# Optimization experiments

Measured on AMD Instinct MI355X. Metric: run time of the kernel, lower is better.

The kernel has to match this reference:

```python
import jax, jax.numpy as jnp
import numpy as np

GROUPS = 32
EPS = 1e-5

def setup_inputs() -> dict:
    key = jax.random.key(0)
    ks = jax.random.split(key, 3)
    b, c, h, w = 4, 256, 64, 64
    x = jax.random.normal(ks[0], (b, c, h, w), dtype=jnp.float32)
    gn_w = jnp.ones((c,), jnp.float32)
    gn_b = jnp.zeros((c,), jnp.float32)
    qkv_w = jax.random.normal(ks[1], (3 * c, c), jnp.float32) * (1.0 / np.sqrt(c))
    qkv_b = jnp.zeros((3 * c,), jnp.float32)
    out_w = jax.random.normal(ks[2], (c, c), jnp.float32) * (1.0 / np.sqrt(c))
    out_b = jnp.zeros((c,), jnp.float32)
    return {"x": x, "gn_w": gn_w, "gn_b": gn_b, "qkv_w": qkv_w,
            "qkv_b": qkv_b, "out_w": out_w, "out_b": out_b}

def reference(x, gn_w, gn_b, qkv_w, qkv_b, out_w, out_b):
    b, c, h, w = x.shape
    scale = c ** (-0.5)
    # GroupNorm over (c/groups, h, w) per group, per-channel affine
    xg = x.reshape(b, GROUPS, c // GROUPS, h, w)
    mean = xg.mean(axis=(2, 3, 4), keepdims=True)
    var = xg.var(axis=(2, 3, 4), keepdims=True)
    xn = ((xg - mean) * jax.lax.rsqrt(var + EPS)).reshape(b, c, h, w)
    xn = xn * gn_w[None, :, None, None] + gn_b[None, :, None, None]
    # 1x1 conv to qkv: [b,3c,h,w]
    qkv = jnp.einsum('bchw,oc->bohw', xn, qkv_w) + qkv_b[None, :, None, None]
    q, k, v = jnp.split(qkv, 3, axis=1)
    # hw_to_seq: [b,c,h,w] -> [b, n, c]
    to_seq = lambda t: t.reshape(b, c, h * w).transpose(0, 2, 1)
    q, k, v = to_seq(q), to_seq(k), to_seq(v)
    sim = jnp.einsum('bic,bjc->bij', q, k) * scale  # [b,n,n]
    attn = jax.nn.softmax(sim, axis=-1)
    out = jnp.einsum('bij,bjc->bic', attn, v)  # [b,n,c]
    out = out.transpose(0, 2, 1).reshape(b, c, h, w)
    out = jnp.einsum('bchw,oc->bohw', out, out_w) + out_b[None, :, None, None]
    return out + x
```

## Files before the change

kernel.cpp:

```cpp
#include <hip/hip_runtime.h>
#include <hip/hip_bf16.h>
#include <stdint.h>

typedef __attribute__((ext_vector_type(8))) short bf16x8;
typedef __attribute__((ext_vector_type(4))) float f32x4;
typedef __attribute__((ext_vector_type(16))) float f32x16;

typedef __attribute__((address_space(1))) const uint32_t gu32;
typedef __attribute__((address_space(3))) uint32_t lu32;

#define N_PIX 4096
#define C_CH  256
#define KVB   128
#define SCALE_LOG2E (0.0625f * 1.4426950408889634f)

__device__ __forceinline__ unsigned short f2bf(float f) {
    unsigned int u = __float_as_uint(f);
    unsigned int r = (u + 0x7FFFu + ((u >> 16) & 1u)) >> 16;
    return (unsigned short)r;
}
__device__ __forceinline__ float bf2f(short s) {
    return __uint_as_float(((unsigned int)(unsigned short)s) << 16);
}

__global__ void prep_kernel(const float* __restrict__ x,
                            const float* __restrict__ gn_w,
                            const float* __restrict__ gn_b,
                            const float* __restrict__ qkv_w,
                            const float* __restrict__ out_w,
                            float* __restrict__ a_out,
                            float* __restrict__ b_out,
                            unsigned short* __restrict__ wq,
                            unsigned short* __restrict__ w2) {
    int bid = blockIdx.x;
    if (bid >= 128) {
        int i = (bid - 128) * 256 + threadIdx.x;
        wq[i] = f2bf(qkv_w[i]);
        if (i < 65536) w2[i] = f2bf(out_w[i]);
        return;
    }
    int b = bid >> 5, g = bid & 31;
    const float* base = x + ((size_t)(b * C_CH + g * 8)) * N_PIX;
    float s1 = 0.f, s2 = 0.f;
    for (int i = threadIdx.x; i < 8 * N_PIX; i += 256) {
        float v = base[i];
        s1 += v; s2 += v * v;
    }
    __shared__ float r1[256], r2[256];
    r1[threadIdx.x] = s1; r2[threadIdx.x] = s2;
    __syncthreads();
    for (int off = 128; off > 0; off >>= 1) {
        if (threadIdx.x < off) {
            r1[threadIdx.x] += r1[threadIdx.x + off];
            r2[threadIdx.x] += r2[threadIdx.x + off];
        }
        __syncthreads();
    }
    if (threadIdx.x < 8) {
        float mean = r1[0] * (1.f / 32768.f);
        float var  = r2[0] * (1.f / 32768.f) - mean * mean;
        float rstd = rsqrtf(var + 1e-5f);
        int c = g * 8 + threadIdx.x;
        float A = rstd * gn_w[c];
        a_out[b * C_CH + c] = A;
        b_out[b * C_CH + c] = gn_b[c] - mean * A;
    }
}

__global__ __launch_bounds__(256)
void qkv_gemm_kernel(const float* __restrict__ x,
                     const float* __restrict__ a_arr,
                     const float* __restrict__ bb_arr,
                     const unsigned short* __restrict__ wq,
                     const float* __restrict__ qkv_b,
                     unsigned short* __restrict__ q_seq,
                     unsigned short* __restrict__ k_seq,
                     unsigned short* __restrict__ vT) {
    __shared__ char wlds[2][16384];
    int pb   = blockIdx.x;
    int och  = blockIdx.y;
    int b    = blockIdx.z;
    int tid  = threadIdx.x;
    int wave = tid >> 6;
    int lane = tid & 63;
    int lo = lane & 15, hi = lane >> 4;
    int prow = pb * 64 + wave * 16 + lo;
    const float* xb = x + (size_t)b * C_CH * N_PIX;
    const float* av = a_arr + b * C_CH;
    const float* bv = bb_arr + b * C_CH;

    auto stageW = [&](int buf, int ks) {
#pragma unroll
        for (int pass = 0; pass < 4; pass++) {
            int chunk = pass * 256 + tid;
            int r = chunk >> 2, cslot = chunk & 3;
            const char* src = (const char*)wq + (size_t)(och * 256 + r) * 512
                              + ks * 64 + cslot * 16;
            __builtin_amdgcn_global_load_lds((gu32*)src,
                                             (lu32*)(wlds[buf] + chunk * 16), 16, 0, 0);
        }
    };

    f32x4 acc[16];
#pragma unroll
    for (int t = 0; t < 16; t++) acc[t] = (f32x4)0.f;

    stageW(0, 0);
    __syncthreads();

#pragma unroll
    for (int ks = 0; ks < 8; ks++) {
        int buf = ks & 1;
        if (ks < 7) stageW(buf ^ 1, ks + 1);
        int c0 = ks * 32 + hi * 8;
        bf16x8 afrag;
#pragma unroll
        for (int i = 0; i < 8; i++) {
            float xv = xb[(size_t)(c0 + i) * N_PIX + prow];
            float v  = fmaf(av[c0 + i], xv, bv[c0 + i]);
            afrag[i] = (short)f2bf(v);
        }
#pragma unroll
        for (int t = 0; t < 16; t++) {
            bf16x8 bfrag = *(const bf16x8*)(wlds[buf] + (t * 16 + lo) * 64 + hi * 16);
            acc[t] = __builtin_amdgcn_mfma_f32_16x16x32_bf16(afrag, bfrag, acc[t], 0, 0, 0);
        }
        __syncthreads();
    }

    int p_base = pb * 64 + wave * 16 + hi * 4;
#pragma unroll
    for (int t = 0; t < 16; t++) {
        int o = och * 256 + t * 16 + lo;
        float bias = qkv_b[o];
        if (och == 2) {
            ushort4 pk;
            pk.x = f2bf(acc[t][0] + bias);
            pk.y = f2bf(acc[t][1] + bias);
            pk.z = f2bf(acc[t][2] + bias);
            pk.w = f2bf(acc[t][3] + bias);
            *(ushort4*)(vT + ((size_t)(b * C_CH + (o - 512))) * N_PIX + p_base) = pk;
        } else {
            float sc = (och == 0) ? SCALE_LOG2E : 1.f;
            unsigned short* dst = (och == 0 ? q_seq : k_seq) + (size_t)b * N_PIX * C_CH;
            int cc = o - och * 256;
#pragma unroll
            for (int r = 0; r < 4; r++)
                dst[(size_t)(p_base + r) * 256 + cc] = f2bf((acc[t][r] + bias) * sc);
        }
    }
}

__global__ __launch_bounds__(512, 2)
void attn_kernel(const unsigned short* __restrict__ q_seq,
                 const unsigned short* __restrict__ k_seq,
                 const unsigned short* __restrict__ vT,
                 unsigned short* __restrict__ o_part,
                 float* __restrict__ m_part,
                 float* __restrict__ l_part) {
    extern __shared__ char lds[];
    char* Kt = lds;
    char* Vt = lds + 65536;
    float* Ml = (float*)(lds + 131072);
    float* Ll = (float*)(lds + 132096);

    int bid  = blockIdx.x;
    int work = (bid & 7) * 32 + (bid >> 3);
    int group = work >> 5;
    int b    = group >> 1;
    int half = group & 1;
    int pq   = work & 31;
    int tid = threadIdx.x;
    int wave = tid >> 6, lane = tid & 63;
    int l31 = lane & 31, hi2 = lane >> 5;
    int qg = wave >> 1, kvh = wave & 1;
    int p0 = pq * 128 + qg * 32;

    const unsigned short* qb = q_seq + (size_t)b * N_PIX * C_CH;
    const unsigned short* kb = k_seq + (size_t)b * N_PIX * C_CH;
    const unsigned short* vb = vT    + (size_t)b * C_CH * N_PIX;

    int ktrow = tid >> 5, kcol = tid & 31;
    int vtrow = tid >> 4, vcol = tid & 15;

    bf16x8 qf[16];
#pragma unroll
    for (int cs = 0; cs < 16; cs++)
        qf[cs] = *(const bf16x8*)(qb + (size_t)(p0 + l31) * 256 + cs * 16 + hi2 * 8);

    f32x16 oacc[8];
#pragma unroll
    for (int t = 0; t < 8; t++) oacc[t] = (f32x16)0.f;
    float m = -1e30f, lsum = 0.f;

    int kswz = l31 << 4;
    int vswz = (l31 & 15) << 4;

    for (int t = 0; t < 16; t++) {
        if (t) __syncthreads();
        int j0 = half * 2048 + t * KVB;
#pragma unroll
        for (int p = 0; p < 8; p++) {
            int kr = p * 16 + ktrow;
            const char* ksrc = (const char*)(kb + (size_t)(j0 + kr) * 256)
                               + ((kcol ^ (kr & 31)) << 4);
            __builtin_amdgcn_global_load_lds((gu32*)ksrc, (lu32*)(Kt + p * 8192 + tid * 16), 16, 0, 0);
            int vr = p * 32 + vtrow;
            const char* vsrc = (const char*)(vb + (size_t)vr * N_PIX + j0)
                               + ((vcol ^ (vr & 15)) << 4);
            __builtin_amdgcn_global_load_lds((gu32*)vsrc, (lu32*)(Vt + p * 8192 + tid * 16), 16, 0, 0);
        }
        __syncthreads();

#pragma unroll
        for (int sub = 0; sub < 2; sub++) {
            int kvb = kvh * 64 + sub * 32;

            f32x16 sacc = (f32x16)0.f;
#pragma unroll
            for (int cs = 0; cs < 16; cs++) {
                bf16x8 kf = *(const bf16x8*)(Kt + (kvb + l31) * 512 + ((cs * 32 + hi2 * 16) ^ kswz));
                sacc = __builtin_amdgcn_mfma_f32_32x32x16_bf16(kf, qf[cs], sacc, 0, 0, 0);
            }

            float mx = sacc[0];
#pragma unroll
            for (int r = 1; r < 16; r++) mx = fmaxf(mx, sacc[r]);
            mx = fmaxf(mx, __shfl_xor(mx, 32, 64));
            if (__any(mx > m + 8.f)) {
                float mC = fmaxf(m, mx);
                float al = __builtin_amdgcn_exp2f(m - mC);
                m = mC; lsum *= al;
#pragma unroll
                for (int r = 0; r < 16; r++) {
                    int qr = (r & 3) + 8 * (r >> 2) + 4 * hi2;
                    float ar = __shfl(al, qr, 64);
#pragma unroll
                    for (int ct = 0; ct < 8; ct++) oacc[ct][r] *= ar;
                }
            }
            f32x16 pexp;
            float psum = 0.f;
#pragma unroll
            for (int r = 0; r < 16; r++) {
                float pe = __builtin_amdgcn_exp2f(sacc[r] - m);
                pexp[r] = pe; psum += pe;
            }
            psum += __shfl_xor(psum, 32, 64);
            lsum += psum;

            bf16x8 pa0, pa1;
            {
                unsigned int x0, x1, y0, y1;
                asm("v_cvt_pk_bf16_f32 %0, %1, %2" : "=v"(x0) : "v"(pexp[0]), "v"(pexp[1]));
                asm("v_cvt_pk_bf16_f32 %0, %1, %2" : "=v"(x1) : "v"(pexp[2]), "v"(pexp[3]));
                asm("v_cvt_pk_bf16_f32 %0, %1, %2" : "=v"(y0) : "v"(pexp[4]), "v"(pexp[5]));
                asm("v_cvt_pk_bf16_f32 %0, %1, %2" : "=v"(y1) : "v"(pexp[6]), "v"(pexp[7]));
                asm("v_permlane32_swap_b32 %0, %1" : "+v"(x0), "+v"(y0));
                asm("v_permlane32_swap_b32 %0, %1" : "+v"(x1), "+v"(y1));
                union { unsigned int u[4]; bf16x8 v; } f0;
                f0.u[0] = x0; f0.u[1] = x1; f0.u[2] = y0; f0.u[3] = y1;
                pa0 = f0.v;
                asm("v_cvt_pk_bf16_f32 %0, %1, %2" : "=v"(x0) : "v"(pexp[8]), "v"(pexp[9]));
                asm("v_cvt_pk_bf16_f32 %0, %1, %2" : "=v"(x1) : "v"(pexp[10]), "v"(pexp[11]));
                asm("v_cvt_pk_bf16_f32 %0, %1, %2" : "=v"(y0) : "v"(pexp[12]), "v"(pexp[13]));
                asm("v_cvt_pk_bf16_f32 %0, %1, %2" : "=v"(y1) : "v"(pexp[14]), "v"(pexp[15]));
                asm("v_permlane32_swap_b32 %0, %1" : "+v"(x0), "+v"(y0));
                asm("v_permlane32_swap_b32 %0, %1" : "+v"(x1), "+v"(y1));
                union { unsigned int u[4]; bf16x8 v; } f1;
                f1.u[0] = x0; f1.u[1] = x1; f1.u[2] = y0; f1.u[3] = y1;
                pa1 = f1.v;
            }

#pragma unroll
            for (int ct = 0; ct < 8; ct++) {
                int c = ct * 32 + l31;
                bf16x8 vf0 = *(const bf16x8*)(Vt + c * 256 + ((kvb * 2 + hi2 * 16) ^ vswz));
                oacc[ct] = __builtin_amdgcn_mfma_f32_32x32x16_bf16(pa0, vf0, oacc[ct], 0, 0, 0);
                bf16x8 vf1 = *(const bf16x8*)(Vt + c * 256 + ((kvb * 2 + 32 + hi2 * 16) ^ vswz));
                oacc[ct] = __builtin_amdgcn_mfma_f32_32x32x16_bf16(pa1, vf1, oacc[ct], 0, 0, 0);
            }
        }
    }
    __syncthreads();

    char* Ow = lds + wave * 16384;
#pragma unroll
    for (int ct = 0; ct < 8; ct++) {
#pragma unroll
        for (int r = 0; r < 16; r++) {
            int q = (r & 3) + 8 * (r >> 2) + 4 * hi2;
            int cb = (ct * 32 + l31) * 2;
            *(unsigned short*)(Ow + q * 512 + (cb ^ (q << 4))) = f2bf(oacc[ct][r]);
        }
    }
    if (lane < 32) { Ml[wave * 32 + lane] = m; Ll[wave * 32 + lane] = lsum; }
    __syncthreads();

    int ql = tid >> 2;
    int qr = ql & 31, qg2 = ql >> 5;
    float g[2];
    float m0 = Ml[(qg2 * 2 + 0) * 32 + qr];
    float m1 = Ml[(qg2 * 2 + 1) * 32 + qr];
    float mm = fmaxf(m0, m1);
    g[0] = __builtin_amdgcn_exp2f(m0 - mm);
    g[1] = __builtin_amdgcn_exp2f(m1 - mm);
    float ls = g[0] * Ll[(qg2 * 2 + 0) * 32 + qr] + g[1] * Ll[(qg2 * 2 + 1) * 32 + qr];
    int qglob = pq * 128 + ql;
    size_t pbase = (size_t)(half * 4 + b) * N_PIX;
    if ((tid & 3) == 0) {
        m_part[pbase + qglob] = mm;
        l_part[pbase + qglob] = ls;
    }
    unsigned short* orow = o_part + (pbase + qglob) * C_CH;
#pragma unroll
    for (int i = 0; i < 8; i++) {
        int s = i * 4 + (tid & 3);
        int cb = (s * 16) ^ (qr << 4);
        bf16x8 a0 = *(const bf16x8*)(lds + (size_t)(qg2 * 2 + 0) * 16384 + qr * 512 + cb);
        bf16x8 a1 = *(const bf16x8*)(lds + (size_t)(qg2 * 2 + 1) * 16384 + qr * 512 + cb);
        union { unsigned short u[8]; bf16x8 v; } pk;
#pragma unroll
        for (int j = 0; j < 8; j++)
            pk.u[j] = f2bf(g[0] * bf2f(a0[j]) + g[1] * bf2f(a1[j]));
        *(bf16x8*)(orow + s * 8) = pk.v;
    }
}

__global__ __launch_bounds__(256)
void combine_kernel(const unsigned short* __restrict__ o_part,
                    const float* __restrict__ m_part,
                    const float* __restrict__ l_part,
                    const unsigned short* __restrict__ w2,
                    const float* __restrict__ out_b,
                    const float* __restrict__ x,
                    float* __restrict__ y) {
    int bid = blockIdx.x;
    int b = bid >> 7, pr = bid & 127;
    int tid = threadIdx.x;
    int wave = tid >> 6, lane = tid & 63;
    int lo = lane & 15, hi = lane >> 4;
    int rowgrp = wave & 1, ohalf = wave >> 1;
    int p0 = pr * 32 + rowgrp * 16;
    int row = p0 + lo;
    size_t i0 = (size_t)b * N_PIX + row;
    size_t i1 = (size_t)(4 + b) * N_PIX + row;
    float m0 = m_part[i0], l0 = l_part[i0];
    float m1 = m_part[i1], l1 = l_part[i1];
    float mm = fmaxf(m0, m1);
    float e0 = __builtin_amdgcn_exp2f(m0 - mm), e1 = __builtin_amdgcn_exp2f(m1 - mm);
    float rl = 1.f / (l0 * e0 + l1 * e1);
    float f0 = e0 * rl, f1 = e1 * rl;
    const unsigned short* P0 = o_part + i0 * C_CH;
    const unsigned short* P1 = o_part + i1 * C_CH;

    f32x4 acc2[8];
#pragma unroll
    for (int t = 0; t < 8; t++) acc2[t] = (f32x4)0.f;

#pragma unroll
    for (int ks = 0; ks < 8; ks++) {
        int c0 = ks * 32 + hi * 8;
        bf16x8 a0 = *(const bf16x8*)(P0 + c0);
        bf16x8 a1 = *(const bf16x8*)(P1 + c0);
        bf16x8 of;
#pragma unroll
        for (int i = 0; i < 8; i++)
            of[i] = (short)f2bf(bf2f(a0[i]) * f0 + bf2f(a1[i]) * f1);
#pragma unroll
        for (int ot = 0; ot < 8; ot++) {
            int o = ohalf * 128 + ot * 16 + lo;
            bf16x8 wf = *(const bf16x8*)(w2 + (size_t)o * 256 + c0);
            acc2[ot] = __builtin_amdgcn_mfma_f32_16x16x32_bf16(of, wf, acc2[ot], 0, 0, 0);
        }
    }

    int p_base = p0 + hi * 4;
#pragma unroll
    for (int ot = 0; ot < 8; ot++) {
        int o = ohalf * 128 + ot * 16 + lo;
        float bias = out_b[o];
        size_t off = ((size_t)(b * C_CH + o)) * N_PIX + p_base;
        f32x4 xv = *(const f32x4*)(x + off);
        f32x4 outv;
#pragma unroll
        for (int r = 0; r < 4; r++) outv[r] = acc2[ot][r] + bias + xv[r];
        *(f32x4*)(y + off) = outv;
    }
}

extern "C" void kernel_launch(void* const* d_in, const int* in_sizes, int n_in,
                              void* d_out, int out_size, void* d_ws, size_t ws_size,
                              hipStream_t stream) {
    const float* x     = (const float*)d_in[0];
    const float* gn_w  = (const float*)d_in[1];
    const float* gn_b  = (const float*)d_in[2];
    const float* qkv_w = (const float*)d_in[3];
    const float* qkv_b = (const float*)d_in[4];
    const float* out_w = (const float*)d_in[5];
    const float* out_b = (const float*)d_in[6];
    float* y = (float*)d_out;
    char* ws = (char*)d_ws;

    float* a_arr  = (float*)(ws);
    float* bb_arr = (float*)(ws + 4096);
    unsigned short* wq     = (unsigned short*)(ws + 8192);
    unsigned short* w2     = (unsigned short*)(ws + 401408);
    unsigned short* q_seq  = (unsigned short*)(ws + 532480);
    unsigned short* k_seq  = (unsigned short*)(ws + 532480 + 8388608);
    unsigned short* vT     = (unsigned short*)(ws + 532480 + 2 * 8388608);
    unsigned short* o_part = (unsigned short*)(ws + 532480 + 3 * 8388608);
    float* m_part = (float*)(ws + 42475520);
    float* l_part = (float*)(ws + 42606592);

    (void)hipFuncSetAttribute((const void*)attn_kernel,
                              hipFuncAttributeMaxDynamicSharedMemorySize, 133120);

    prep_kernel<<<896, 256, 0, stream>>>(x, gn_w, gn_b, qkv_w, out_w,
                                         a_arr, bb_arr, wq, w2);
    qkv_gemm_kernel<<<dim3(64, 3, 4), 256, 0, stream>>>(x, a_arr, bb_arr, wq, qkv_b,
                                                        q_seq, k_seq, vT);
    attn_kernel<<<256, 512, 133120, stream>>>(q_seq, k_seq, vT, o_part, m_part, l_part);
    combine_kernel<<<512, 256, 0, stream>>>(o_part, m_part, l_part, w2, out_b, x, y);
}
```

Baseline: 173.0 us.

## Split attention KV into four quarters with 64-key tiles and halved LDS

The attention kernel now splits the 4096 keys into four quarters instead of two, so it launches 512 blocks instead of 256. Each iteration loads a 64-key tile, which halves LDS use to about 66KB and can allow more resident blocks per CU. The two KV-half waves now merge their partial outputs inside LDS before writing a single o_part row. The combine kernel then reduces four partials instead of two. This trades more intermediate traffic and combine work for better occupancy and more parallelism. The V tile addressing is remapped to fit the smaller tile.

```diff
diff --git a/kernel.cpp b/kernel.cpp
--- a/kernel.cpp
+++ b/kernel.cpp
@@ -11,7 +11,6 @@
 
 #define N_PIX 4096
 #define C_CH  256
-#define KVB   128
 #define SCALE_LOG2E (0.0625f * 1.4426950408889634f)
 
 __device__ __forceinline__ unsigned short f2bf(float f) {
@@ -160,29 +159,27 @@
                  float* __restrict__ l_part) {
     extern __shared__ char lds[];
     char* Kt = lds;
-    char* Vt = lds + 65536;
-    float* Ml = (float*)(lds + 131072);
-    float* Ll = (float*)(lds + 132096);
+    char* Vt = lds + 32768;
+    float* Ml = (float*)(lds + 65536);
+    float* Ll = (float*)(lds + 66560);
 
     int bid  = blockIdx.x;
-    int work = (bid & 7) * 32 + (bid >> 3);
+    int work = (bid & 7) * 64 + (bid >> 3);
     int group = work >> 5;
-    int b    = group >> 1;
-    int half = group & 1;
-    int pq   = work & 31;
+    int b   = group >> 2;
+    int qtr = group & 3;
+    int pq  = work & 31;
     int tid = threadIdx.x;
     int wave = tid >> 6, lane = tid & 63;
     int l31 = lane & 31, hi2 = lane >> 5;
     int qg = wave >> 1, kvh = wave & 1;
     int p0 = pq * 128 + qg * 32;
+    int kvb = kvh * 32;
 
     const unsigned short* qb = q_seq + (size_t)b * N_PIX * C_CH;
     const unsigned short* kb = k_seq + (size_t)b * N_PIX * C_CH;
     const unsigned short* vb = vT    + (size_t)b * C_CH * N_PIX;
 
-    int ktrow = tid >> 5, kcol = tid & 31;
-    int vtrow = tid >> 4, vcol = tid & 15;
-
     bf16x8 qf[16];
 #pragma unroll
     for (int cs = 0; cs < 16; cs++)
@@ -194,136 +191,154 @@
     float m = -1e30f, lsum = 0.f;
 
     int kswz = l31 << 4;
-    int vswz = (l31 & 15) << 4;
 
     for (int t = 0; t < 16; t++) {
         if (t) __syncthreads();
-        int j0 = half * 2048 + t * KVB;
-#pragma unroll
-        for (int p = 0; p < 8; p++) {
-            int kr = p * 16 + ktrow;
-            const char* ksrc = (const char*)(kb + (size_t)(j0 + kr) * 256)
-                               + ((kcol ^ (kr & 31)) << 4);
-            __builtin_amdgcn_global_load_lds((gu32*)ksrc, (lu32*)(Kt + p * 8192 + tid * 16), 16, 0, 0);
-            int vr = p * 32 + vtrow;
-            const char* vsrc = (const char*)(vb + (size_t)vr * N_PIX + j0)
-                               + ((vcol ^ (vr & 15)) << 4);
-            __builtin_amdgcn_global_load_lds((gu32*)vsrc, (lu32*)(Vt + p * 8192 + tid * 16), 16, 0, 0);
+        int j0 = qtr * 1024 + t * 64;
+        const char* kjb = (const char*)kb + (size_t)j0 * 512;
+        const char* vjb = (const char*)vb + (size_t)j0 * 2;
+#pragma unroll
+        for (int p = 0; p < 4; p++) {
+            int kr = p * 16 + (tid >> 5);
+            int ks = tid & 31;
+            __builtin_amdgcn_global_load_lds(
+                (gu32*)(kjb + kr * 512 + ((ks ^ (kr & 31)) << 4)),
+                (lu32*)(Kt + p * 8192 + tid * 16), 16, 0, 0);
+            int vr = p * 32 + (tid >> 4);
+            int vs = tid & 15;
+            int tt = vs ^ (vr & 15);
+            int c  = 2 * vr + (tt >> 3);
+            __builtin_amdgcn_global_load_lds(
+                (gu32*)(vjb + (size_t)c * 8192 + ((tt & 7) << 4)),
+                (lu32*)(Vt + p * 8192 + tid * 16), 16, 0, 0);
         }
         __syncthreads();
 
-#pragma unroll
-        for (int sub = 0; sub < 2; sub++) {
-            int kvb = kvh * 64 + sub * 32;
-
-            f32x16 sacc = (f32x16)0.f;
-#pragma unroll
-            for (int cs = 0; cs < 16; cs++) {
-                bf16x8 kf = *(const bf16x8*)(Kt + (kvb + l31) * 512 + ((cs * 32 + hi2 * 16) ^ kswz));
-                sacc = __builtin_amdgcn_mfma_f32_32x32x16_bf16(kf, qf[cs], sacc, 0, 0, 0);
+        f32x16 sacc = (f32x16)0.f;
+#pragma unroll
+        for (int cs = 0; cs < 16; cs++) {
+            bf16x8 kf = *(const bf16x8*)(Kt + (kvb + l31) * 512 + ((cs * 32 + hi2 * 16) ^ kswz));
+            sacc = __builtin_amdgcn_mfma_f32_32x32x16_bf16(kf, qf[cs], sacc, 0, 0, 0);
+        }
+
+        float mx = sacc[0];
+#pragma unroll
+        for (int r = 1; r < 16; r++) mx = fmaxf(mx, sacc[r]);
+        mx = fmaxf(mx, __shfl_xor(mx, 32, 64));
+        if (__any(mx > m + 8.f)) {
+            float mC = fmaxf(m, mx);
+            float al = __builtin_amdgcn_exp2f(m - mC);
+            m = mC; lsum *= al;
+#pragma unroll
+            for (int r = 0; r < 16; r++) {
+                int qr = (r & 3) + 8 * (r >> 2) + 4 * hi2;
+                float ar = __shfl(al, qr, 64);
+#pragma unroll
+                for (int ct = 0; ct < 8; ct++) oacc[ct][r] *= ar;
             }
-
-            float mx = sacc[0];
-#pragma unroll
-            for (int r = 1; r < 16; r++) mx = fmaxf(mx, sacc[r]);
-            mx = fmaxf(mx, __shfl_xor(mx, 32, 64));
-            if (__any(mx > m + 8.f)) {
-                float mC = fmaxf(m, mx);
-                float al = __builtin_amdgcn_exp2f(m - mC);
-                m = mC; lsum *= al;
-#pragma unroll
-                for (int r = 0; r < 16; r++) {
-                    int qr = (r & 3) + 8 * (r >> 2) + 4 * hi2;
-                    float ar = __shfl(al, qr, 64);
-#pragma unroll
-                    for (int ct = 0; ct < 8; ct++) oacc[ct][r] *= ar;
-                }
+        }
+        f32x16 pexp;
+        float psum = 0.f;
+#pragma unroll
+        for (int r = 0; r < 16; r++) {
+            float pe = __builtin_amdgcn_exp2f(sacc[r] - m);
+            pexp[r] = pe; psum += pe;
+        }
+        psum += __shfl_xor(psum, 32, 64);
+        lsum += psum;
+
+        bf16x8 pa0, pa1;
+        {
+            unsigned int x0, x1, y0, y1;
+            asm("v_cvt_pk_bf16_f32 %0, %1, %2" : "=v"(x0) : "v"(pexp[0]), "v"(pexp[1]));
+            asm("v_cvt_pk_bf16_f32 %0, %1, %2" : "=v"(x1) : "v"(pexp[2]), "v"(pexp[3]));
+            asm("v_cvt_pk_bf16_f32 %0, %1, %2" : "=v"(y0) : "v"(pexp[4]), "v"(pexp[5]));
+            asm("v_cvt_pk_bf16_f32 %0, %1, %2" : "=v"(y1) : "v"(pexp[6]), "v"(pexp[7]));
+            asm("v_permlane32_swap_b32 %0, %1" : "+v"(x0), "+v"(y0));
+            asm("v_permlane32_swap_b32 %0, %1" : "+v"(x1), "+v"(y1));
+            union { unsigned int u[4]; bf16x8 v; } f0;
+            f0.u[0] = x0; f0.u[1] = x1; f0.u[2] = y0; f0.u[3] = y1;
+            pa0 = f0.v;
+            asm("v_cvt_pk_bf16_f32 %0, %1, %2" : "=v"(x0) : "v"(pexp[8]), "v"(pexp[9]));
+            asm("v_cvt_pk_bf16_f32 %0, %1, %2" : "=v"(x1) : "v"(pexp[10]), "v"(pexp[11]));
+            asm("v_cvt_pk_bf16_f32 %0, %1, %2" : "=v"(y0) : "v"(pexp[12]), "v"(pexp[13]));
+            asm("v_cvt_pk_bf16_f32 %0, %1, %2" : "=v"(y1) : "v"(pexp[14]), "v"(pexp[15]));
+            asm("v_permlane32_swap_b32 %0, %1" : "+v"(x0), "+v"(y0));
+            asm("v_permlane32_swap_b32 %0, %1" : "+v"(x1), "+v"(y1));
+            union { unsigned int u[4]; bf16x8 v; } f1;
+            f1.u[0] = x0; f1.u[1] = x1; f1.u[2] = y0; f1.u[3] = y1;
+            pa1 = f1.v;
+        }
+
+#pragma unroll
+        for (int ct = 0; ct < 8; ct++) {
+            int c = ct * 32 + l31;
+            int vrow = c >> 1;
+            int s0i = (c & 1) * 8 + kvh * 4 + hi2;
+            bf16x8 vf0 = *(const bf16x8*)(Vt + vrow * 256 + ((s0i ^ (vrow & 15)) << 4));
+            oacc[ct] = __builtin_amdgcn_mfma_f32_32x32x16_bf16(pa0, vf0, oacc[ct], 0, 0, 0);
+            int s1i = s0i + 2;
+            bf16x8 vf1 = *(const bf16x8*)(Vt + vrow * 256 + ((s1i ^ (vrow & 15)) << 4));
+            oacc[ct] = __builtin_amdgcn_mfma_f32_32x32x16_bf16(pa1, vf1, oacc[ct], 0, 0, 0);
+        }
+    }
+    __syncthreads();
+
+    if (lane < 32) { Ml[wave * 32 + lane] = m; Ll[wave * 32 + lane] = lsum; }
+    if (kvh == 0) {
+        char* Ow = lds + qg * 16384;
+#pragma unroll
+        for (int ct = 0; ct < 8; ct++)
+#pragma unroll
+            for (int r = 0; r < 16; r++) {
+                int q = (r & 3) + 8 * (r >> 2) + 4 * hi2;
+                int cb = (ct * 32 + l31) * 2;
+                *(unsigned short*)(Ow + q * 512 + (cb ^ (q << 4))) = f2bf(oacc[ct][r]);
             }
-            f32x16 pexp;
-            float psum = 0.f;
+    }
+    __syncthreads();
+    size_t pbase = (size_t)(qtr * 4 + b) * N_PIX;
+    if (kvh == 1) {
+        char* Ow = lds + qg * 16384;
+        float mp = Ml[(wave - 1) * 32 + l31], lp = Ll[(wave - 1) * 32 + l31];
+        float mn = fmaxf(m, mp);
+        float fo = __builtin_amdgcn_exp2f(m - mn);
+        float fp = __builtin_amdgcn_exp2f(mp - mn);
+        float lm = lsum * fo + lp * fp;
+        if (lane < 32) {
+            m_part[pbase + p0 + l31] = mn;
+            l_part[pbase + p0 + l31] = lm;
+        }
+        float FO[16], FP[16];
+#pragma unroll
+        for (int r = 0; r < 16; r++) {
+            int qr = (r & 3) + 8 * (r >> 2) + 4 * hi2;
+            FO[r] = __shfl(fo, qr, 64);
+            FP[r] = __shfl(fp, qr, 64);
+        }
+#pragma unroll
+        for (int ct = 0; ct < 8; ct++)
 #pragma unroll
             for (int r = 0; r < 16; r++) {
-                float pe = __builtin_amdgcn_exp2f(sacc[r] - m);
-                pexp[r] = pe; psum += pe;
+                int q = (r & 3) + 8 * (r >> 2) + 4 * hi2;
+                int cb = (ct * 32 + l31) * 2;
+                unsigned short* ad = (unsigned short*)(Ow + q * 512 + (cb ^ (q << 4)));
+                float mg = bf2f((short)*ad) * FP[r] + oacc[ct][r] * FO[r];
+                *ad = f2bf(mg);
             }
-            psum += __shfl_xor(psum, 32, 64);
-            lsum += psum;
-
-            bf16x8 pa0, pa1;
-            {
-                unsigned int x0, x1, y0, y1;
-                asm("v_cvt_pk_bf16_f32 %0, %1, %2" : "=v"(x0) : "v"(pexp[0]), "v"(pexp[1]));
-                asm("v_cvt_pk_bf16_f32 %0, %1, %2" : "=v"(x1) : "v"(pexp[2]), "v"(pexp[3]));
-                asm("v_cvt_pk_bf16_f32 %0, %1, %2" : "=v"(y0) : "v"(pexp[4]), "v"(pexp[5]));
-                asm("v_cvt_pk_bf16_f32 %0, %1, %2" : "=v"(y1) : "v"(pexp[6]), "v"(pexp[7]));
-                asm("v_permlane32_swap_b32 %0, %1" : "+v"(x0), "+v"(y0));
-                asm("v_permlane32_swap_b32 %0, %1" : "+v"(x1), "+v"(y1));
-                union { unsigned int u[4]; bf16x8 v; } f0;
-                f0.u[0] = x0; f0.u[1] = x1; f0.u[2] = y0; f0.u[3] = y1;
-                pa0 = f0.v;
-                asm("v_cvt_pk_bf16_f32 %0, %1, %2" : "=v"(x0) : "v"(pexp[8]), "v"(pexp[9]));
-                asm("v_cvt_pk_bf16_f32 %0, %1, %2" : "=v"(x1) : "v"(pexp[10]), "v"(pexp[11]));
-                asm("v_cvt_pk_bf16_f32 %0, %1, %2" : "=v"(y0) : "v"(pexp[12]), "v"(pexp[13]));
-                asm("v_cvt_pk_bf16_f32 %0, %1, %2" : "=v"(y1) : "v"(pexp[14]), "v"(pexp[15]));
-                asm("v_permlane32_swap_b32 %0, %1" : "+v"(x0), "+v"(y0));
-                asm("v_permlane32_swap_b32 %0, %1" : "+v"(x1), "+v"(y1));
-                union { unsigned int u[4]; bf16x8 v; } f1;
-                f1.u[0] = x0; f1.u[1] = x1; f1.u[2] = y0; f1.u[3] = y1;
-                pa1 = f1.v;
-            }
-
-#pragma unroll
-            for (int ct = 0; ct < 8; ct++) {
-                int c = ct * 32 + l31;
-                bf16x8 vf0 = *(const bf16x8*)(Vt + c * 256 + ((kvb * 2 + hi2 * 16) ^ vswz));
-                oacc[ct] = __builtin_amdgcn_mfma_f32_32x32x16_bf16(pa0, vf0, oacc[ct], 0, 0, 0);
-                bf16x8 vf1 = *(const bf16x8*)(Vt + c * 256 + ((kvb * 2 + 32 + hi2 * 16) ^ vswz));
-                oacc[ct] = __builtin_amdgcn_mfma_f32_32x32x16_bf16(pa1, vf1, oacc[ct], 0, 0, 0);
-            }
-        }
     }
     __syncthreads();
-
-    char* Ow = lds + wave * 16384;
-#pragma unroll
-    for (int ct = 0; ct < 8; ct++) {
-#pragma unroll
-        for (int r = 0; r < 16; r++) {
-            int q = (r & 3) + 8 * (r >> 2) + 4 * hi2;
-            int cb = (ct * 32 + l31) * 2;
-            *(unsigned short*)(Ow + q * 512 + (cb ^ (q << 4))) = f2bf(oacc[ct][r]);
-        }
-    }
-    if (lane < 32) { Ml[wave * 32 + lane] = m; Ll[wave * 32 + lane] = lsum; }
-    __syncthreads();
-
-    int ql = tid >> 2;
-    int qr = ql & 31, qg2 = ql >> 5;
-    float g[2];
-    float m0 = Ml[(qg2 * 2 + 0) * 32 + qr];
-    float m1 = Ml[(qg2 * 2 + 1) * 32 + qr];
-    float mm = fmaxf(m0, m1);
-    g[0] = __builtin_amdgcn_exp2f(m0 - mm);
-    g[1] = __builtin_amdgcn_exp2f(m1 - mm);
-    float ls = g[0] * Ll[(qg2 * 2 + 0) * 32 + qr] + g[1] * Ll[(qg2 * 2 + 1) * 32 + qr];
-    int qglob = pq * 128 + ql;
-    size_t pbase = (size_t)(half * 4 + b) * N_PIX;
-    if ((tid & 3) == 0) {
-        m_part[pbase + qglob] = mm;
-        l_part[pbase + qglob] = ls;
-    }
-    unsigned short* orow = o_part + (pbase + qglob) * C_CH;
-#pragma unroll
-    for (int i = 0; i < 8; i++) {
-        int s = i * 4 + (tid & 3);
-        int cb = (s * 16) ^ (qr << 4);
-        bf16x8 a0 = *(const bf16x8*)(lds + (size_t)(qg2 * 2 + 0) * 16384 + qr * 512 + cb);
-        bf16x8 a1 = *(const bf16x8*)(lds + (size_t)(qg2 * 2 + 1) * 16384 + qr * 512 + cb);
-        union { unsigned short u[8]; bf16x8 v; } pk;
-#pragma unroll
-        for (int j = 0; j < 8; j++)
-            pk.u[j] = f2bf(g[0] * bf2f(a0[j]) + g[1] * bf2f(a1[j]));
-        *(bf16x8*)(orow + s * 8) = pk.v;
+    {
+        int ql = tid >> 2;
+        int qr = ql & 31, qg2 = ql >> 5;
+        unsigned short* orow = o_part + (pbase + pq * 128 + ql) * C_CH;
+#pragma unroll
+        for (int i = 0; i < 8; i++) {
+            int s = i * 4 + (tid & 3);
+            int cb = (s * 16) ^ (qr << 4);
+            bf16x8 v = *(const bf16x8*)(lds + (size_t)qg2 * 16384 + qr * 512 + cb);
+            *(bf16x8*)(orow + s * 8) = v;
+        }
     }
 }
 
@@ -343,16 +358,24 @@
     int rowgrp = wave & 1, ohalf = wave >> 1;
     int p0 = pr * 32 + rowgrp * 16;
     int row = p0 + lo;
-    size_t i0 = (size_t)b * N_PIX + row;
-    size_t i1 = (size_t)(4 + b) * N_PIX + row;
-    float m0 = m_part[i0], l0 = l_part[i0];
-    float m1 = m_part[i1], l1 = l_part[i1];
-    float mm = fmaxf(m0, m1);
-    float e0 = __builtin_amdgcn_exp2f(m0 - mm), e1 = __builtin_amdgcn_exp2f(m1 - mm);
-    float rl = 1.f / (l0 * e0 + l1 * e1);
-    float f0 = e0 * rl, f1 = e1 * rl;
-    const unsigned short* P0 = o_part + i0 * C_CH;
-    const unsigned short* P1 = o_part + i1 * C_CH;
+    size_t idx[4];
+    float mk[4], lk[4];
+    float mm = -1e30f;
+#pragma unroll
+    for (int k = 0; k < 4; k++) {
+        idx[k] = (size_t)(k * 4 + b) * N_PIX + row;
+        mk[k] = m_part[idx[k]]; lk[k] = l_part[idx[k]];
+        mm = fmaxf(mm, mk[k]);
+    }
+    float fsum = 0.f, fk[4];
+#pragma unroll
+    for (int k = 0; k < 4; k++) {
+        fk[k] = __builtin_amdgcn_exp2f(mk[k] - mm);
+        fsum += fk[k] * lk[k];
+    }
+    float rl = 1.f / fsum;
+#pragma unroll
+    for (int k = 0; k < 4; k++) fk[k] *= rl;
 
     f32x4 acc2[8];
 #pragma unroll
@@ -361,12 +384,15 @@
 #pragma unroll
     for (int ks = 0; ks < 8; ks++) {
         int c0 = ks * 32 + hi * 8;
-        bf16x8 a0 = *(const bf16x8*)(P0 + c0);
-        bf16x8 a1 = *(const bf16x8*)(P1 + c0);
+        bf16x8 a0 = *(const bf16x8*)(o_part + idx[0] * C_CH + c0);
+        bf16x8 a1 = *(const bf16x8*)(o_part + idx[1] * C_CH + c0);
+        bf16x8 a2 = *(const bf16x8*)(o_part + idx[2] * C_CH + c0);
+        bf16x8 a3 = *(const bf16x8*)(o_part + idx[3] * C_CH + c0);
         bf16x8 of;
 #pragma unroll
         for (int i = 0; i < 8; i++)
-            of[i] = (short)f2bf(bf2f(a0[i]) * f0 + bf2f(a1[i]) * f1);
+            of[i] = (short)f2bf(fk[0] * bf2f(a0[i]) + fk[1] * bf2f(a1[i]) +
+                                fk[2] * bf2f(a2[i]) + fk[3] * bf2f(a3[i]));
 #pragma unroll
         for (int ot = 0; ot < 8; ot++) {
             int o = ohalf * 128 + ot * 16 + lo;
@@ -410,16 +436,16 @@
     unsigned short* k_seq  = (unsigned short*)(ws + 532480 + 8388608);
     unsigned short* vT     = (unsigned short*)(ws + 532480 + 2 * 8388608);
     unsigned short* o_part = (unsigned short*)(ws + 532480 + 3 * 8388608);
-    float* m_part = (float*)(ws + 42475520);
-    float* l_part = (float*)(ws + 42606592);
+    float* m_part = (float*)(ws + 59252736);
+    float* l_part = (float*)(ws + 59514880);
 
     (void)hipFuncSetAttribute((const void*)attn_kernel,
-                              hipFuncAttributeMaxDynamicSharedMemorySize, 133120);
+                              hipFuncAttributeMaxDynamicSharedMemorySize, 67584);
 
     prep_kernel<<<896, 256, 0, stream>>>(x, gn_w, gn_b, qkv_w, out_w,
                                          a_arr, bb_arr, wq, w2);
     qkv_gemm_kernel<<<dim3(64, 3, 4), 256, 0, stream>>>(x, a_arr, bb_arr, wq, qkv_b,
                                                         q_seq, k_seq, vT);
-    attn_kernel<<<256, 512, 133120, stream>>>(q_seq, k_seq, vT, o_part, m_part, l_part);
+    attn_kernel<<<512, 512, 67584, stream>>>(q_seq, k_seq, vT, o_part, m_part, l_part);
     combine_kernel<<<512, 256, 0, stream>>>(o_part, m_part, l_part, w2, out_b, x, y);
 }
```

After: 203.6 us. +17.6%, slower.
